# Performance work log

Hardware: AMD Instinct MI355X
Metric: run time of the kernel (lower is better)

## Reference

```python
import jax, jax.numpy as jnp
import numpy as np

WIRES = 24
DIMS = [2] * WIRES
INDEX = [0, 2, 3, 4, 5, 6, 7, 8, 9, 10, 11]  # control = wire 0, targets = wires 2..11
D_CONTROL = DIMS[INDEX[0]]                   # 2
D_TARGET = int(np.prod([DIMS[i] for i in INDEX[1:]]))  # 1024
REMAINING = [i for i in range(WIRES) if i not in INDEX]
D_REM = int(np.prod([DIMS[i] for i in REMAINING])) if REMAINING else 1  # 8192
NEW_ORDER = INDEX + REMAINING
INV_ORDER = [NEW_ORDER.index(i) for i in range(WIRES)]
N = int(np.prod(DIMS))  # 2**24


def setup_inputs() -> dict:
    key = jax.random.key(0)
    k1, k2, k3, k4 = jax.random.split(key, 4)
    return {
        "x_real": jax.random.normal(k1, (N,), dtype=jnp.float32),
        "x_imag": jax.random.normal(k2, (N,), dtype=jnp.float32),
        "U_real": jax.random.normal(k3, (D_CONTROL, D_TARGET, D_TARGET), dtype=jnp.float32),
        "U_imag": jax.random.normal(k4, (D_CONTROL, D_TARGET, D_TARGET), dtype=jnp.float32),
    }


def reference(x_real, x_imag, U_real, U_imag):
    x = (x_real + 1j * x_imag).astype(jnp.complex64)
    A = (U_real + 1j * U_imag).astype(jnp.complex64)  # [d_c, d_t, d_t]
    # Skew-Hermitian generator -> unitary blocks via batched matrix exponential
    skew = A - jnp.conj(jnp.swapaxes(A, -1, -2))
    U_blocks = jax.vmap(jax.scipy.linalg.expm)(skew)  # [d_c, d_t, d_t]

    # Bring control + target wires to the front
    st = x.reshape(DIMS).transpose(NEW_ORDER)          # [2]*wires permuted
    A_blk = st.reshape(D_CONTROL, D_TARGET, D_REM)     # [d_c, d_t, d_rem]

    # Block-diagonal unitary applied as a batched per-control matmul
    out = jnp.einsum('ktd,kdr->ktr', U_blocks, A_blk)  # [d_c, d_t, d_rem]

    new_shape = ([D_CONTROL] + [DIMS[i] for i in INDEX[1:]]
                 + ([DIMS[i] for i in REMAINING] if REMAINING else []))
    state_new = out.reshape(new_shape).transpose(INV_ORDER).reshape(-1, 1)
    # Return as stacked (real, imag) float32 since the state is complex64
    return jnp.stack([state_new.real, state_new.imag])  # [2, N, 1]
```

## Files before the change

kernel.cpp:

```cpp
#include <hip/hip_runtime.h>
#include <hip/hip_bf16.h>

#define PLANE (1 << 20)

typedef __attribute__((ext_vector_type(8))) short bf16x8;
typedef __attribute__((ext_vector_type(4))) float f32x4;

struct SegOff { long o[6]; };

union U4 { ushort u[4]; unsigned long long v; };

__device__ __forceinline__ ushort bf16bits(float v) {
    union { __hip_bfloat16 b; ushort u; } c;
    c.b = __float2bfloat16(v);
    return c.u;
}

__device__ __forceinline__ void split2(float v, ushort& hi, ushort& lo) {
    union { __hip_bfloat16 b; ushort u; } c;
    __hip_bfloat16 h = __float2bfloat16(v);
    c.b = h; hi = c.u;
    c.b = __float2bfloat16(v - __bfloat162float(h));
    lo = c.u;
}

__device__ __forceinline__ void gload16(const ushort* g, ushort* l) {
    __builtin_amdgcn_global_load_lds(
        (const __attribute__((address_space(1))) unsigned int*)g,
        (__attribute__((address_space(3))) unsigned int*)l, 16, 0, 0);
}

__global__ __launch_bounds__(256) void build_skew_k(
    const float* __restrict__ Ure, const float* __restrict__ Uim,
    float* __restrict__ Bre, float* __restrict__ Bim, float scale)
{
    int idx = blockIdx.x * 256 + threadIdx.x;
    int ij  = idx & (PLANE - 1);
    int i   = ij >> 10, j = ij & 1023;
    int t   = (idx & ~(PLANE - 1)) | (j << 10) | i;
    Bre[idx] = (Ure[idx] - Ure[t]) * scale;
    Bim[idx] = (Uim[idx] + Uim[t]) * scale;
}

__global__ __launch_bounds__(256) void init_T_k(
    const float* __restrict__ Bre, const float* __restrict__ Bim,
    float* __restrict__ Tre, float* __restrict__ Tim, float inv)
{
    int idx = blockIdx.x * 256 + threadIdx.x;
    int ij  = idx & (PLANE - 1);
    int i   = ij >> 10, j = ij & 1023;
    Tre[idx] = Bre[idx] * inv + ((i == j) ? 1.0f : 0.0f);
    Tim[idx] = Bim[idx] * inv;
}

__global__ __launch_bounds__(256) void reduce_k(
    float* __restrict__ C, const float* __restrict__ PB, float scale, int addI)
{
    long e = ((long)blockIdx.x * 256 + threadIdx.x) * 4;
    float4 v = *(float4*)(C + e);
    const float4 a = *(const float4*)(PB + e);
    const float4 b = *(const float4*)(PB + 4L * PLANE + e);
    const float4 c = *(const float4*)(PB + 8L * PLANE + e);
    v.x = (v.x + a.x + b.x + c.x) * scale;
    v.y = (v.y + a.y + b.y + c.y) * scale;
    v.z = (v.z + a.z + b.z + c.z) * scale;
    v.w = (v.w + a.w + b.w + c.w) * scale;
    if (addI) {
        long p = e >> 20;
        if (p < 2) {
            int ij = (int)(e & (PLANE - 1));
            int i = ij >> 10, j = ij & 1023;
            if (i >= j && i < j + 4) ((float*)&v)[i - j] += 1.0f;
        }
    }
    *(float4*)(C + e) = v;
}

__global__ __launch_bounds__(256) void pack_A6_k(
    const float* __restrict__ Sre, const float* __restrict__ Sim,
    ushort* __restrict__ Ab)
{
    int idx = blockIdx.x * 256 + threadIdx.x;
    int k   = idx >> 18;
    int m   = (idx >> 8) & 1023;
    int c4  = (idx & 255) * 4;
    const float4 vr = *(const float4*)(Sre + (size_t)k * PLANE + (size_t)m * 1024 + c4);
    const float4 vi = *(const float4*)(Sim + (size_t)k * PLANE + (size_t)m * 1024 + c4);
    U4 rh, rl, ih, il, nih, nil;
    split2(vr.x, rh.u[0], rl.u[0]); split2(vr.y, rh.u[1], rl.u[1]);
    split2(vr.z, rh.u[2], rl.u[2]); split2(vr.w, rh.u[3], rl.u[3]);
    split2(vi.x, ih.u[0], il.u[0]); split2(vi.y, ih.u[1], il.u[1]);
    split2(vi.z, ih.u[2], il.u[2]); split2(vi.w, ih.u[3], il.u[3]);
    #pragma unroll
    for (int i = 0; i < 4; ++i) { nih.u[i] = ih.u[i] ^ 0x8000; nil.u[i] = il.u[i] ^ 0x8000; }

    long b0 = (long)k * 1024 * 6144 + (long)m * 6144;
    long b1 = (long)(2 + k) * 1024 * 6144 + (long)m * 6144;
    *(unsigned long long*)&Ab[b0 + 0*1024 + c4] = rh.v;
    *(unsigned long long*)&Ab[b0 + 1*1024 + c4] = rh.v;
    *(unsigned long long*)&Ab[b0 + 2*1024 + c4] = rl.v;
    *(unsigned long long*)&Ab[b0 + 3*1024 + c4] = nih.v;
    *(unsigned long long*)&Ab[b0 + 4*1024 + c4] = nih.v;
    *(unsigned long long*)&Ab[b0 + 5*1024 + c4] = nil.v;
    *(unsigned long long*)&Ab[b1 + 0*1024 + c4] = ih.v;
    *(unsigned long long*)&Ab[b1 + 1*1024 + c4] = ih.v;
    *(unsigned long long*)&Ab[b1 + 2*1024 + c4] = il.v;
    *(unsigned long long*)&Ab[b1 + 3*1024 + c4] = rh.v;
    *(unsigned long long*)&Ab[b1 + 4*1024 + c4] = rh.v;
    *(unsigned long long*)&Ab[b1 + 5*1024 + c4] = rl.v;
}

__global__ __launch_bounds__(256) void pack_A4_k(
    const float* __restrict__ Sre, const float* __restrict__ Sim,
    ushort* __restrict__ Ab)
{
    int idx = blockIdx.x * 256 + threadIdx.x;
    int k   = idx >> 18;
    int m   = (idx >> 8) & 1023;
    int c4  = (idx & 255) * 4;
    const float4 vr = *(const float4*)(Sre + (size_t)k * PLANE + (size_t)m * 1024 + c4);
    const float4 vi = *(const float4*)(Sim + (size_t)k * PLANE + (size_t)m * 1024 + c4);
    U4 rh, rl, ih, il, nih, nil;
    split2(vr.x, rh.u[0], rl.u[0]); split2(vr.y, rh.u[1], rl.u[1]);
    split2(vr.z, rh.u[2], rl.u[2]); split2(vr.w, rh.u[3], rl.u[3]);
    split2(vi.x, ih.u[0], il.u[0]); split2(vi.y, ih.u[1], il.u[1]);
    split2(vi.z, ih.u[2], il.u[2]); split2(vi.w, ih.u[3], il.u[3]);
    #pragma unroll
    for (int i = 0; i < 4; ++i) { nih.u[i] = ih.u[i] ^ 0x8000; nil.u[i] = il.u[i] ^ 0x8000; }

    long b0 = (long)k * 1024 * 4096 + (long)m * 4096;
    long b1 = (long)(2 + k) * 1024 * 4096 + (long)m * 4096;
    *(unsigned long long*)&Ab[b0 + 0*1024 + c4] = rh.v;
    *(unsigned long long*)&Ab[b0 + 1*1024 + c4] = rl.v;
    *(unsigned long long*)&Ab[b0 + 2*1024 + c4] = nih.v;
    *(unsigned long long*)&Ab[b0 + 3*1024 + c4] = nil.v;
    *(unsigned long long*)&Ab[b1 + 0*1024 + c4] = ih.v;
    *(unsigned long long*)&Ab[b1 + 1*1024 + c4] = il.v;
    *(unsigned long long*)&Ab[b1 + 2*1024 + c4] = rh.v;
    *(unsigned long long*)&Ab[b1 + 3*1024 + c4] = rl.v;
}

__global__ __launch_bounds__(256) void pack_BT6_k(
    const float* __restrict__ Sre, const float* __restrict__ Sim,
    ushort* __restrict__ Tt)
{
    __shared__ float Lre[64][65];
    __shared__ float Lim[64][65];
    int k = blockIdx.z, r0 = blockIdx.y * 64, c0 = blockIdx.x * 64;
    int tid = threadIdx.x;
    const float* br = Sre + (size_t)k * PLANE;
    const float* bi = Sim + (size_t)k * PLANE;
    #pragma unroll
    for (int p = 0; p < 16; ++p) {
        int idx = p * 256 + tid, r = idx >> 6, c = idx & 63;
        Lre[r][c] = br[(size_t)(r0 + r) * 1024 + c0 + c];
        Lim[r][c] = bi[(size_t)(r0 + r) * 1024 + c0 + c];
    }
    __syncthreads();
    #pragma unroll
    for (int p = 0; p < 4; ++p) {
        int s = p * 256 + tid, oc = s >> 4, r4 = (s & 15) * 4;
        U4 rh, rl, ih, il;
        #pragma unroll
        for (int i = 0; i < 4; ++i) {
            split2(Lre[r4 + i][oc], rh.u[i], rl.u[i]);
            split2(Lim[r4 + i][oc], ih.u[i], il.u[i]);
        }
        size_t dst = (size_t)k * PLANE + (size_t)(c0 + oc) * 1024 + r0 + r4;
        *(unsigned long long*)&Tt[0L * 2 * PLANE + dst] = rh.v;
        *(unsigned long long*)&Tt[1L * 2 * PLANE + dst] = rl.v;
        *(unsigned long long*)&Tt[2L * 2 * PLANE + dst] = ih.v;
        *(unsigned long long*)&Tt[3L * 2 * PLANE + dst] = il.v;
    }
}

__global__ __launch_bounds__(256) void pack_xT_k(
    const float* __restrict__ xre, const float* __restrict__ xim,
    ushort* __restrict__ xT)
{
    __shared__ float Lre[64][65];
    __shared__ float Lim[64][65];
    int pl = blockIdx.z, t0 = blockIdx.y * 64, c0 = blockIdx.x * 64;
    int tid = threadIdx.x;
    const float* br = xre + ((size_t)pl << 22);
    const float* bi = xim + ((size_t)pl << 22);
    #pragma unroll
    for (int p = 0; p < 16; ++p) {
        int idx = p * 256 + tid, r = idx >> 6, c = idx & 63;
        Lre[r][c] = br[(size_t)(t0 + r) * 4096 + c0 + c];
        Lim[r][c] = bi[(size_t)(t0 + r) * 4096 + c0 + c];
    }
    __syncthreads();
    #pragma unroll
    for (int p = 0; p < 4; ++p) {
        int s = p * 256 + tid, oc = s >> 4, r4 = (s & 15) * 4;
        U4 re4, im4;
        #pragma unroll
        for (int i = 0; i < 4; ++i) {
            re4.u[i] = bf16bits(Lre[r4 + i][oc]);
            im4.u[i] = bf16bits(Lim[r4 + i][oc]);
        }
        size_t dst = ((size_t)pl << 22) + (size_t)(c0 + oc) * 1024 + t0 + r4;
        *(unsigned long long*)&xT[dst] = re4.v;
        *(unsigned long long*)&xT[(4L << 22) + dst] = im4.v;
    }
}

__global__ __launch_bounds__(512, 2) void gemm256_k(
    const ushort* __restrict__ Ab, long aPackStride, long aInnerStride, int aInnerDiv, int aLd,
    const ushort* __restrict__ Bb, SegOff segs, long bZStride,
    float* __restrict__ CreB, float* __restrict__ CimB, long cZStride, int cLd,
    int kLen, int zHalf, float scale, int addI,
    float* __restrict__ PB)
{
    __shared__ ushort lds[2][32768];

    const int zTot  = 2 * zHalf;
    const int chunk = blockIdx.z / zTot;
    const int zb    = blockIdx.z % zTot;
    const int pack  = zb / zHalf, inner = zb % zHalf;
    const ushort* A = Ab + (long)pack * aPackStride + (long)(inner / aInnerDiv) * aInnerStride;
    float* C = (chunk == 0)
        ? ((pack ? CimB : CreB) + (long)inner * cZStride)
        : (PB + (long)(chunk - 1) * 4 * PLANE + (long)pack * 2 * PLANE + (long)inner * PLANE);

    const int tid  = threadIdx.x;
    const int lane = tid & 63, wave = tid >> 6;
    const int wr = wave >> 2, wc = wave & 3;
    const int l15 = lane & 15, quad = lane >> 4;
    const int m0 = blockIdx.y * 256, n0 = blockIdx.x * 256;

    const int srow  = lane >> 3;
    const int scolE = ((((lane & 7) * 16) ^ (((lane >> 5) & 1) << 5)) >> 1);
    const int xorv  = ((l15 >> 2) & 1) << 5;
    const int abase = ((((wr * 128 + l15) * 128 + quad * 16) ^ xorv) >> 1);
    const int bbase = ((((wc * 64  + l15) * 128 + quad * 16) ^ xorv) >> 1);

    const int kStart = chunk * kLen;
    const int nt = kLen >> 6;

    f32x4 acc[8][4] = {};

#define STAGE(T, BUF)                                                          \
    {                                                                          \
        int kb_ = kStart + (T) * 64;                                           \
        const ushort* Ag_ = A + (long)m0 * aLd + kb_;                          \
        const ushort* Bg_ = Bb + segs.o[kb_ >> 10] + (long)inner * bZStride    \
                            + (long)n0 * 1024 + (kb_ & 1023);                  \
        ushort* lA_ = &lds[BUF][0];                                            \
        ushort* lB_ = &lds[BUF][16384];                                        \
        _Pragma("unroll")                                                      \
        for (int i_ = 0; i_ < 4; ++i_) {                                       \
            int br_ = (wave * 4 + i_) * 8 + srow;                              \
            gload16(Ag_ + (long)br_ * aLd + scolE, lA_ + (wave * 4 + i_) * 512); \
            gload16(Bg_ + (long)br_ * 1024 + scolE, lB_ + (wave * 4 + i_) * 512); \
        }                                                                      \
    }

#define PHASE(MQ, KQ, LOADB)                                                   \
    {                                                                          \
        if (LOADB) {                                                           \
            _Pragma("unroll")                                                  \
            for (int j_ = 0; j_ < 4; ++j_)                                     \
                bfr[j_] = *(const bf16x8*)&lB[bbase + j_ * 1024 + (KQ) * 32];  \
        }                                                                      \
        bf16x8 aa[4];                                                          \
        _Pragma("unroll")                                                      \
        for (int i_ = 0; i_ < 4; ++i_)                                         \
            aa[i_] = *(const bf16x8*)&lA[abase + ((MQ) * 4 + i_) * 1024 + (KQ) * 32]; \
        asm volatile("s_barrier" ::: "memory");                                \
        __builtin_amdgcn_s_setprio(1);                                         \
        _Pragma("unroll")                                                      \
        for (int i_ = 0; i_ < 4; ++i_) {                                       \
            _Pragma("unroll")                                                  \
            for (int j_ = 0; j_ < 4; ++j_)                                     \
                acc[(MQ) * 4 + i_][j_] = __builtin_amdgcn_mfma_f32_16x16x32_bf16( \
                    aa[i_], bfr[j_], acc[(MQ) * 4 + i_][j_], 0, 0, 0);         \
        }                                                                      \
        __builtin_amdgcn_s_setprio(0);                                         \
        asm volatile("s_barrier" ::: "memory");                                \
    }

    STAGE(0, 0);
    STAGE(1, 1);

    for (int t = 0; t < nt; ++t) {
        ushort* lA = &lds[t & 1][0];
        ushort* lB = &lds[t & 1][16384];
        if (t + 1 < nt) { asm volatile("s_waitcnt vmcnt(8)" ::: "memory"); }
        else            { asm volatile("s_waitcnt vmcnt(0)" ::: "memory"); }
        asm volatile("s_barrier" ::: "memory");
        bf16x8 bfr[4];
        PHASE(0, 0, 1);
        PHASE(1, 0, 0);
        PHASE(0, 1, 1);
        PHASE(1, 1, 0);
        if (t + 2 < nt) STAGE(t + 2, t & 1);
    }
#undef PHASE
#undef STAGE

    #pragma unroll
    for (int fm = 0; fm < 8; ++fm) {
        int row0 = m0 + wr * 128 + fm * 16 + quad * 4;
        #pragma unroll
        for (int fn = 0; fn < 4; ++fn) {
            int col = n0 + wc * 64 + fn * 16 + l15;
            #pragma unroll
            for (int r = 0; r < 4; ++r) {
                float v = acc[fm][fn][r] * scale;
                if (addI && chunk == 0 && pack == 0 && (row0 + r) == col) v += 1.0f;
                C[(long)(row0 + r) * cLd + col] = v;
            }
        }
    }
}

extern "C" void kernel_launch(void* const* d_in, const int* in_sizes, int n_in,
                              void* d_out, int out_size, void* d_ws, size_t ws_size,
                              hipStream_t stream)
{
    const float* x_re = (const float*)d_in[0];
    const float* x_im = (const float*)d_in[1];
    const float* U_re = (const float*)d_in[2];
    const float* U_im = (const float*)d_in[3];
    float* out = (float*)d_out;

    float* fp = (float*)d_ws;
    float* Tre = fp + 0L * 2 * PLANE;
    float* Tim = fp + 1L * 2 * PLANE;
    float* Rre = fp + 2L * 2 * PLANE;
    float* Rim = fp + 3L * 2 * PLANE;
    float* BSre = fp + 4L * 2 * PLANE;
    float* BSim = fp + 5L * 2 * PLANE;
    ushort* Askew = (ushort*)((char*)d_ws + (48L << 20));
    ushort* At    = (ushort*)((char*)d_ws + (96L << 20));
    ushort* Tt    = (ushort*)((char*)d_ws + (144L << 20));
    ushort* Aap   = Askew;
    ushort* xT    = At;
    float* Phorner = (float*)At;
    float* Psquare = (float*)Askew;

    dim3 blk(256);
    dim3 blk5(512);

    const float scaleB = 1.0f / 512.0f;
    build_skew_k<<<dim3(2 * PLANE / 256), blk, 0, stream>>>(U_re, U_im, BSre, BSim, scaleB);
    init_T_k<<<dim3(2 * PLANE / 256), blk, 0, stream>>>(BSre, BSim, Tre, Tim, 1.0f / 8.0f);
    pack_A6_k<<<dim3(2048), blk, 0, stream>>>(BSre, BSim, Askew);

    SegOff se;
    se.o[0] = 0L;           se.o[1] = 2L * PLANE;  se.o[2] = 0L;
    se.o[3] = 4L * PLANE;   se.o[4] = 6L * PLANE;  se.o[5] = 4L * PLANE;

    dim3 ge(4, 4, 16);
    dim3 gr(PLANE / 256);
    for (int j = 7; j >= 1; --j) {
        pack_BT6_k<<<dim3(16, 16, 2), blk, 0, stream>>>(Tre, Tim, Tt);
        gemm256_k<<<ge, blk5, 0, stream>>>(Askew, 2L * 1024 * 6144, 1024L * 6144, 1, 6144,
                                           Tt, se, (long)PLANE,
                                           Rre, Rim, (long)PLANE, 1024,
                                           1536, 2, 1.0f, 0, Phorner);
        reduce_k<<<gr, blk, 0, stream>>>(Rre, Phorner, 1.0f / (float)j, 1);
        float* t;
        t = Tre; Tre = Rre; Rre = t;
        t = Tim; Tim = Rim; Rim = t;
    }
    for (int s = 0; s < 9; ++s) {
        pack_A6_k<<<dim3(2048), blk, 0, stream>>>(Tre, Tim, At);
        pack_BT6_k<<<dim3(16, 16, 2), blk, 0, stream>>>(Tre, Tim, Tt);
        gemm256_k<<<ge, blk5, 0, stream>>>(At, 2L * 1024 * 6144, 1024L * 6144, 1, 6144,
                                           Tt, se, (long)PLANE,
                                           Rre, Rim, (long)PLANE, 1024,
                                           1536, 2, 1.0f, 0, Psquare);
        reduce_k<<<gr, blk, 0, stream>>>(Rre, Psquare, 1.0f, 0);
        float* t;
        t = Tre; Tre = Rre; Rre = t;
        t = Tim; Tim = Rim; Rim = t;
    }

    pack_A4_k<<<dim3(2048), blk, 0, stream>>>(Tre, Tim, Aap);
    pack_xT_k<<<dim3(64, 16, 4), blk, 0, stream>>>(x_re, x_im, xT);

    SegOff sa;
    sa.o[0] = 0L;        sa.o[1] = 0L;
    sa.o[2] = 4L << 22;  sa.o[3] = 4L << 22;
    sa.o[4] = 0L;        sa.o[5] = 0L;

    gemm256_k<<<dim3(16, 4, 8), blk5, 0, stream>>>(Aap, 2L * 1024 * 4096, 1024L * 4096, 2, 4096,
                                                   xT, sa, 1L << 22,
                                                   out, out + (1L << 24), 1L << 22, 4096,
                                                   4096, 4, 1.0f, 0, (float*)nullptr);
}
```

Baseline: 2.246 ms.

## Interleave global-to-LDS loads across MFMA phases with per-K-half staging

Restructures the GEMM main loop so each 64-wide K tile is staged in two 32-wide halves, and the global-to-LDS loads for the next tile are spread across the four MFMA phases instead of issued in one burst. The LDS layout and swizzle also change to a 32-element row layout with an XOR swizzle on 8-element groups. Waits become finer-grained vmcnt(4) fences placed per phase, and the last iteration redundantly reloads the final tile rather than branching. This aims to hide load latency better and smooth out memory issue. The price is extra loads on the final iteration and the risk of new LDS bank conflicts or a subtle race from the changed wait counts.

```diff
diff --git a/kernel.cpp b/kernel.cpp
--- a/kernel.cpp
+++ b/kernel.cpp
@@ -230,44 +230,50 @@
     const int l15 = lane & 15, quad = lane >> 4;
     const int m0 = blockIdx.y * 256, n0 = blockIdx.x * 256;
 
-    const int srow  = lane >> 3;
-    const int scolE = ((((lane & 7) * 16) ^ (((lane >> 5) & 1) << 5)) >> 1);
-    const int xorv  = ((l15 >> 2) & 1) << 5;
-    const int abase = ((((wr * 128 + l15) * 128 + quad * 16) ^ xorv) >> 1);
-    const int bbase = ((((wc * 64  + l15) * 128 + quad * 16) ^ xorv) >> 1);
+    const int r0s  = tid >> 2;
+    const int r1s  = 128 + r0s;
+    const int scol = ((tid & 3) ^ ((tid >> 2) & 3)) * 8;
+    const int dU0  = tid * 8;
+    const int dU1  = 4096 + tid * 8;
+    const int swzE  = (quad * 8) ^ ((l15 & 3) << 3);
+    const int aBase = wr * 4096 + l15 * 32 + swzE;
+    const int bBase = wc * 2048 + l15 * 32 + swzE;
 
     const int kStart = chunk * kLen;
     const int nt = kLen >> 6;
 
     f32x4 acc[8][4] = {};
 
-#define STAGE(T, BUF)                                                          \
+#define STAGE_A(KQ, T, BUF)                                                    \
     {                                                                          \
         int kb_ = kStart + (T) * 64;                                           \
-        const ushort* Ag_ = A + (long)m0 * aLd + kb_;                          \
-        const ushort* Bg_ = Bb + segs.o[kb_ >> 10] + (long)inner * bZStride    \
-                            + (long)n0 * 1024 + (kb_ & 1023);                  \
-        ushort* lA_ = &lds[BUF][0];                                            \
-        ushort* lB_ = &lds[BUF][16384];                                        \
-        _Pragma("unroll")                                                      \
-        for (int i_ = 0; i_ < 4; ++i_) {                                       \
-            int br_ = (wave * 4 + i_) * 8 + srow;                              \
-            gload16(Ag_ + (long)br_ * aLd + scolE, lA_ + (wave * 4 + i_) * 512); \
-            gload16(Bg_ + (long)br_ * 1024 + scolE, lB_ + (wave * 4 + i_) * 512); \
-        }                                                                      \
-    }
-
-#define PHASE(MQ, KQ, LOADB)                                                   \
+        const ushort* g_ = A + kb_ + (KQ) * 32 + scol;                         \
+        ushort* d_ = &lds[BUF][(KQ) * 8192];                                   \
+        gload16(g_ + (long)(m0 + r0s) * aLd, d_ + dU0);                        \
+        gload16(g_ + (long)(m0 + r1s) * aLd, d_ + dU1);                        \
+    }
+#define STAGE_B(KQ, T, BUF)                                                    \
+    {                                                                          \
+        int kb_ = kStart + (T) * 64;                                           \
+        const ushort* g_ = Bb + segs.o[kb_ >> 10] + (long)inner * bZStride     \
+                           + (kb_ & 1023) + (KQ) * 32 + scol;                  \
+        ushort* d_ = &lds[BUF][16384 + (KQ) * 8192];                           \
+        gload16(g_ + (long)(n0 + r0s) * 1024, d_ + dU0);                       \
+        gload16(g_ + (long)(n0 + r1s) * 1024, d_ + dU1);                       \
+    }
+
+#define PHASE(MQ, KQ, LOADB, STAGE_STMT, VMFENCE)                              \
     {                                                                          \
         if (LOADB) {                                                           \
             _Pragma("unroll")                                                  \
             for (int j_ = 0; j_ < 4; ++j_)                                     \
-                bfr[j_] = *(const bf16x8*)&lB[bbase + j_ * 1024 + (KQ) * 32];  \
+                bfr[j_] = *(const bf16x8*)&lB[(KQ) * 8192 + bBase + j_ * 512]; \
         }                                                                      \
         bf16x8 aa[4];                                                          \
         _Pragma("unroll")                                                      \
         for (int i_ = 0; i_ < 4; ++i_)                                         \
-            aa[i_] = *(const bf16x8*)&lA[abase + ((MQ) * 4 + i_) * 1024 + (KQ) * 32]; \
+            aa[i_] = *(const bf16x8*)&lA[(KQ) * 8192 + aBase + ((MQ) * 4 + i_) * 512]; \
+        STAGE_STMT;                                                            \
         asm volatile("s_barrier" ::: "memory");                                \
         __builtin_amdgcn_s_setprio(1);                                         \
         _Pragma("unroll")                                                      \
@@ -278,27 +284,30 @@
                     aa[i_], bfr[j_], acc[(MQ) * 4 + i_][j_], 0, 0, 0);         \
         }                                                                      \
         __builtin_amdgcn_s_setprio(0);                                         \
+        VMFENCE;                                                               \
         asm volatile("s_barrier" ::: "memory");                                \
     }
 
-    STAGE(0, 0);
-    STAGE(1, 1);
+    STAGE_A(0, 0, 0); STAGE_B(0, 0, 0); STAGE_A(1, 0, 0); STAGE_B(1, 0, 0);
+    asm volatile("s_waitcnt vmcnt(4)" ::: "memory");
+    asm volatile("s_barrier" ::: "memory");
 
     for (int t = 0; t < nt; ++t) {
-        ushort* lA = &lds[t & 1][0];
-        ushort* lB = &lds[t & 1][16384];
-        if (t + 1 < nt) { asm volatile("s_waitcnt vmcnt(8)" ::: "memory"); }
-        else            { asm volatile("s_waitcnt vmcnt(0)" ::: "memory"); }
-        asm volatile("s_barrier" ::: "memory");
+        const int cur = t & 1, nx = cur ^ 1;
+        const ushort* lA = &lds[cur][0];
+        const ushort* lB = &lds[cur][16384];
+        const int tn = (t + 1 < nt) ? (t + 1) : (nt - 1);
         bf16x8 bfr[4];
-        PHASE(0, 0, 1);
-        PHASE(1, 0, 0);
-        PHASE(0, 1, 1);
-        PHASE(1, 1, 0);
-        if (t + 2 < nt) STAGE(t + 2, t & 1);
+        PHASE(0, 0, 1, STAGE_A(0, tn, nx), );
+        PHASE(1, 0, 0, STAGE_B(0, tn, nx),
+              asm volatile("s_waitcnt vmcnt(4)" ::: "memory"));
+        PHASE(0, 1, 1, STAGE_A(1, tn, nx), );
+        PHASE(1, 1, 0, STAGE_B(1, tn, nx),
+              asm volatile("s_waitcnt vmcnt(4)" ::: "memory"));
     }
 #undef PHASE
-#undef STAGE
+#undef STAGE_A
+#undef STAGE_B
 
     #pragma unroll
     for (int fm = 0; fm < 8; ++fm) {
```

Measured after the change: 1.965 ms. 1.14x faster.
